# Optimization experiments

Measured on AMD Instinct MI355X. Metric: run time of the kernel, lower is better.

## Reference

```python
import jax, jax.numpy as jnp
import numpy as np

BINS = 2048
SCENE = 8
EPS = 1e-8
P_LOW = 2.0
P_HIGH = 100.0


def setup_inputs() -> dict:
    key = jax.random.key(0)
    k1, k2 = jax.random.split(key)
    x = jax.random.uniform(k1, (8, 1, 1024, 1280), dtype=jnp.float32)
    delta = jax.random.normal(k2, (SCENE, BINS), dtype=jnp.float32)
    return {"x": x, "delta": delta}


def reference(x, delta):
    B = x.shape[0]
    if x.shape[1] == 3:
        x = jnp.mean(x, axis=1, keepdims=True)
    # robust per-sample quantile normalization -> [0, 1]
    x_flat = x.reshape(B, -1)
    lo = jnp.quantile(x_flat, P_LOW / 100.0, axis=1).reshape(B, 1, 1, 1)
    hi = jnp.quantile(x_flat, P_HIGH / 100.0, axis=1).reshape(B, 1, 1, 1)
    xn = jnp.clip((x - lo) / (hi - lo + EPS), 0.0, 1.0)
    # uniform scene mixture (scene selector unused in original forward)
    scene_idx = jnp.ones((B, SCENE), dtype=x.dtype) / SCENE
    increments = jax.nn.softplus(scene_idx @ delta) + EPS  # (B, BINS)
    luts = jnp.cumsum(increments, axis=1)
    luts = luts / (luts[:, -1:] + EPS) * 2.0 - 1.0  # monotonic, range ~[-1, 1]
    # per-sample gather: pixel value -> bin index -> LUT value
    idx = jnp.clip((xn * (BINS - 1)).astype(jnp.int32), 0, BINS - 1)  # (B,1,H,W)
    y = jnp.take_along_axis(luts, idx.reshape(B, -1), axis=1).reshape(xn.shape)
    return jnp.tile(y, (1, 3, 1, 1))
```

## Files before the change

kernel.cpp:

```cpp
#include <hip/hip_runtime.h>
#include <hip/hip_bf16.h>
#include <math.h>

#define NB 8
#define HH 1024
#define WW 1280
#define HW (HH*WW)
#define N4 (HW/4)
#define LBINS 2048
#define HBINS 2048
#define NSCENE 8
#define EPSF 1e-8f
#define CAPMAX 8192

typedef float f32x4 __attribute__((ext_vector_type(4)));

#define WS_HIST    0
#define WS_MAXB    (WS_HIST + NB*HBINS)
#define WS_CNT     (WS_MAXB + NB)
#define WS_ZERO_WORDS (WS_CNT + NB)
#define WS_INFO    16400
#define WS_LOHI    (WS_INFO + NB*4)
#define WS_LUT     (WS_LOHI + NB*2)
#define WS_COLLECT 18560

__device__ __forceinline__ unsigned fkey(float f) {
    unsigned u = __float_as_uint(f);
    return (u & 0x80000000u) ? ~u : (u | 0x80000000u);
}
__device__ __forceinline__ float keyf(unsigned k) {
    unsigned u = (k & 0x80000000u) ? (k & 0x7fffffffu) : ~k;
    return __uint_as_float(u);
}

__global__ __launch_bounds__(256) void k_zero(unsigned* __restrict__ ws) {
    int i = blockIdx.x * 256 + threadIdx.x;
    if (i < WS_ZERO_WORDS) ws[i] = 0u;
}

__global__ __launch_bounds__(256) void k_hist(const float* __restrict__ x,
                                              unsigned* __restrict__ ws) {
    __shared__ unsigned lh[HBINS];
    __shared__ float redf[4];
    const int s = blockIdx.y;
    for (int i = threadIdx.x; i < HBINS; i += 256) lh[i] = 0u;
    __syncthreads();
    const float4* xs = (const float4*)(x + (size_t)s * HW);
    float mx = -3.4e38f;
    for (int i = blockIdx.x * 256 + threadIdx.x; i < N4; i += gridDim.x * 256) {
        float4 v = xs[i];
        float fv[4] = {v.x, v.y, v.z, v.w};
#pragma unroll
        for (int c = 0; c < 4; ++c) {
            float f = fv[c];
            int b = (int)(f * 2048.0f);
            b = b < 0 ? 0 : (b > 2047 ? 2047 : b);
            atomicAdd(&lh[b], 1u);
            mx = fmaxf(mx, f);
        }
    }
    for (int d = 32; d > 0; d >>= 1) mx = fmaxf(mx, __shfl_down(mx, d));
    __syncthreads();
    if ((threadIdx.x & 63) == 0) redf[threadIdx.x >> 6] = mx;
    __syncthreads();
    unsigned* gh = ws + WS_HIST + s * HBINS;
    for (int i = threadIdx.x; i < HBINS; i += 256) {
        unsigned c = lh[i];
        if (c) atomicAdd(&gh[i], c);
    }
    if (threadIdx.x == 0) {
        float m2 = fmaxf(fmaxf(redf[0], redf[1]), fmaxf(redf[2], redf[3]));
        atomicMax(&ws[WS_MAXB + s], fkey(m2));
    }
}

__global__ __launch_bounds__(64) void k_scan(unsigned* __restrict__ ws) {
    const int s = blockIdx.x;
    const unsigned* gh = ws + WS_HIST + s * HBINS;
    int lane = threadIdx.x;
    unsigned cnt[32];
    unsigned run = 0u;
#pragma unroll
    for (int i = 0; i < 32; ++i) { cnt[i] = gh[lane * 32 + i]; run += cnt[i]; }
    unsigned xs = run;
    for (int d = 1; d < 64; d <<= 1) {
        unsigned y = __shfl_up(xs, d);
        if (lane >= d) xs += y;
    }
    unsigned before = xs - run;
    const float idxf = 0.02f * (float)(HW - 1);
    const unsigned k = (unsigned)idxf;
#pragma unroll
    for (int i = 0; i < 32; ++i) {
        unsigned c = cnt[i];
        unsigned bin = lane * 32 + i;
        if (before <= k && k < before + c) {
            ws[WS_INFO + s * 4 + 0] = bin;
            ws[WS_INFO + s * 4 + 2] = k - before;
        }
        if (before <= k + 1 && k + 1 < before + c) {
            ws[WS_INFO + s * 4 + 1] = bin;
        }
        before += c;
    }
}

__global__ __launch_bounds__(64) void k_lut(const float* __restrict__ delta,
                                            float* __restrict__ lut) {
    __shared__ float inc[LBINS];
    int lane = threadIdx.x;
    for (int j = lane; j < LBINS; j += 64) {
        float ssum = 0.0f;
#pragma unroll
        for (int sc = 0; sc < NSCENE; ++sc) ssum += delta[sc * LBINS + j];
        float v = ssum * 0.125f;
        inc[j] = fmaxf(v, 0.0f) + log1pf(expf(-fabsf(v))) + EPSF;
    }
    __syncthreads();
    float loc[32];
    float run = 0.0f;
#pragma unroll
    for (int i = 0; i < 32; ++i) { run += inc[lane * 32 + i]; loc[i] = run; }
    float xv = run;
    for (int d = 1; d < 64; d <<= 1) {
        float y = __shfl_up(xv, d);
        if (lane >= d) xv += y;
    }
    float excl = xv - run;
    float total = __shfl(xv, 63);
#pragma unroll
    for (int i = 0; i < 32; ++i) {
        float c = excl + loc[i];
        lut[lane * 32 + i] = c / (total + EPSF) * 2.0f - 1.0f;
    }
}

__global__ __launch_bounds__(256) void k_collect(const float* __restrict__ x,
                                                 unsigned* __restrict__ ws, int cap) {
    const int s = blockIdx.y;
    const unsigned t1 = ws[WS_INFO + s * 4 + 0];
    const unsigned t2 = ws[WS_INFO + s * 4 + 1];
    float* coll = (float*)(ws + WS_COLLECT) + (size_t)s * cap;
    unsigned* cnt = ws + WS_CNT + s;
    const float4* xs = (const float4*)(x + (size_t)s * HW);
    for (int i = blockIdx.x * 256 + threadIdx.x; i < N4; i += gridDim.x * 256) {
        float4 v = xs[i];
        float fv[4] = {v.x, v.y, v.z, v.w};
#pragma unroll
        for (int c = 0; c < 4; ++c) {
            float f = fv[c];
            int b = (int)(f * 2048.0f);
            b = b < 0 ? 0 : (b > 2047 ? 2047 : b);
            if ((unsigned)b >= t1 && (unsigned)b <= t2) {
                unsigned p = atomicAdd(cnt, 1u);
                if (p < (unsigned)cap) coll[p] = f;
            }
        }
    }
}

__global__ __launch_bounds__(256) void k_select(unsigned* __restrict__ ws, int cap) {
    __shared__ unsigned keys[CAPMAX];
    __shared__ unsigned hist[256];
    __shared__ unsigned pfx[256];
    __shared__ unsigned s_bucket, s_r;
    __shared__ unsigned s_L, s_E, s_mg;
    const int s = blockIdx.x;
    const int tid = threadIdx.x;
    unsigned m = ws[WS_CNT + s];
    if (m > (unsigned)cap) m = (unsigned)cap;
    const float* coll = (const float*)(ws + WS_COLLECT) + (size_t)s * cap;
    const unsigned jrel = ws[WS_INFO + s * 4 + 2];

    for (unsigned i = tid; i < m; i += 256) keys[i] = fkey(coll[i]);
    if (tid == 0) { s_L = 0; s_E = 0; s_mg = 0xFFFFFFFFu; }
    __syncthreads();

    unsigned prefix = 0;
    unsigned r = jrel;
    for (int shift = 24; shift >= 0; shift -= 8) {
        hist[tid] = 0u;
        __syncthreads();
        for (unsigned i = tid; i < m; i += 256) {
            unsigned kk = keys[i];
            bool ok = (shift == 24) || ((kk >> (shift + 8)) == prefix);
            if (ok) atomicAdd(&hist[(kk >> shift) & 255u], 1u);
        }
        __syncthreads();
        if (tid < 64) {
            unsigned a0 = hist[tid*4+0], a1 = hist[tid*4+1];
            unsigned a2 = hist[tid*4+2], a3 = hist[tid*4+3];
            unsigned sum = a0 + a1 + a2 + a3;
            unsigned inc = sum;
            for (int d = 1; d < 64; d <<= 1) {
                unsigned y = __shfl_up(inc, d);
                if (tid >= d) inc += y;
            }
            unsigned excl = inc - sum;
            pfx[tid*4+0] = excl;
            pfx[tid*4+1] = excl + a0;
            pfx[tid*4+2] = excl + a0 + a1;
            pfx[tid*4+3] = excl + a0 + a1 + a2;
        }
        __syncthreads();
        {
            unsigned e = pfx[tid], c = hist[tid];
            if (e <= r && r < e + c) { s_bucket = tid; s_r = r - e; }
        }
        __syncthreads();
        prefix = (prefix << 8) | s_bucket;
        r = s_r;
        __syncthreads();
    }
    const unsigned vk = prefix;
    unsigned lL = 0, lE = 0, lmg = 0xFFFFFFFFu;
    for (unsigned i = tid; i < m; i += 256) {
        unsigned kk = keys[i];
        lL += (kk < vk) ? 1u : 0u;
        lE += (kk == vk) ? 1u : 0u;
        if (kk > vk && kk < lmg) lmg = kk;
    }
    atomicAdd(&s_L, lL);
    atomicAdd(&s_E, lE);
    atomicMin(&s_mg, lmg);
    __syncthreads();
    if (tid == 0) {
        unsigned vk1 = (jrel + 1 < s_L + s_E) ? vk : s_mg;
        float svk = keyf(vk), svk1 = keyf(vk1);
        const float idxf = 0.02f * (float)(HW - 1);
        const float frac = idxf - (float)((unsigned)idxf);
        float lo = svk * (1.0f - frac) + svk1 * frac;
        float hi = keyf(ws[WS_MAXB + s]);
        float* lh = (float*)(ws + WS_LOHI);
        lh[s * 2 + 0] = lo;
        lh[s * 2 + 1] = hi;
    }
}

__global__ __launch_bounds__(256) void k_apply(const float* __restrict__ x,
                                               const unsigned* __restrict__ ws,
                                               float* __restrict__ y) {
    __shared__ float slut[LBINS];
    const float* lutg = (const float*)(ws + WS_LUT);
    for (int i = threadIdx.x; i < LBINS; i += 256) slut[i] = lutg[i];
    const int s = blockIdx.y;
    const float* lh = (const float*)(ws + WS_LOHI);
    const float lo = lh[s * 2 + 0];
    const float hi = lh[s * 2 + 1];
    const float denom = hi - lo + EPSF;
    __syncthreads();
    const f32x4* xs = (const f32x4*)(x + (size_t)s * HW);
    f32x4* y0 = (f32x4*)(y + (size_t)s * 3 * HW);
    f32x4* y1 = (f32x4*)(y + (size_t)s * 3 * HW + HW);
    f32x4* y2 = (f32x4*)(y + (size_t)s * 3 * HW + 2 * HW);
    for (int i = blockIdx.x * 256 + threadIdx.x; i < N4; i += gridDim.x * 256) {
        f32x4 v = xs[i];
        f32x4 o;
#pragma unroll
        for (int c = 0; c < 4; ++c) {
            float xn = (v[c] - lo) / denom;
            xn = xn < 0.0f ? 0.0f : (xn > 1.0f ? 1.0f : xn);
            float t = xn * 2047.0f;
            int idx = (int)t;
            idx = idx < 0 ? 0 : (idx > 2047 ? 2047 : idx);
            o[c] = slut[idx];
        }
        __builtin_nontemporal_store(o, &y0[i]);
        __builtin_nontemporal_store(o, &y1[i]);
        __builtin_nontemporal_store(o, &y2[i]);
    }
}

extern "C" void kernel_launch(void* const* d_in, const int* in_sizes, int n_in,
                              void* d_out, int out_size, void* d_ws, size_t ws_size,
                              hipStream_t stream) {
    const float* x = (const float*)d_in[0];
    const float* delta = (const float*)d_in[1];
    float* y = (float*)d_out;
    unsigned* ws = (unsigned*)d_ws;

    int cap = CAPMAX;
    size_t avail_words = ws_size / 4;
    size_t per_sample = avail_words > WS_COLLECT ? (avail_words - WS_COLLECT) / NB : 0;
    if ((size_t)cap > per_sample) cap = (int)per_sample;

    k_zero<<<dim3((WS_ZERO_WORDS + 255) / 256), dim3(256), 0, stream>>>(ws);
    k_hist<<<dim3(64, NB), dim3(256), 0, stream>>>(x, ws);
    k_scan<<<dim3(NB), dim3(64), 0, stream>>>(ws);
    k_lut<<<dim3(1), dim3(64), 0, stream>>>(delta, (float*)(ws + WS_LUT));
    k_collect<<<dim3(32, NB), dim3(256), 0, stream>>>(x, ws, cap);
    k_select<<<dim3(NB), dim3(256), 0, stream>>>(ws, cap);
    k_apply<<<dim3(320, NB), dim3(256), 0, stream>>>(x, ws, y);
}
```

Baseline: 300.4 us.

## Replace global histogram atomics with per-block partials and merge scan/LUT kernels

The histogram kernel now writes a per-block partial histogram and per-block max to workspace instead of atomically adding into a zeroed global histogram. That removes the zeroing kernel and the global atomics. The scan and LUT kernels are fused into one launch with an extra block for the LUT, and that kernel reduces the partials and max and resets the collect counter. The collect grid is doubled. Launch count drops by two, but the scan must now read 64 partial histograms per sample (about 4 MB in total), and the workspace layout grows.

```diff
diff --git a/kernel.cpp b/kernel.cpp
--- a/kernel.cpp
+++ b/kernel.cpp
@@ -12,17 +12,17 @@
 #define NSCENE 8
 #define EPSF 1e-8f
 #define CAPMAX 8192
+#define HBLK 64
 
 typedef float f32x4 __attribute__((ext_vector_type(4)));
 
-#define WS_HIST    0
-#define WS_MAXB    (WS_HIST + NB*HBINS)
-#define WS_CNT     (WS_MAXB + NB)
-#define WS_ZERO_WORDS (WS_CNT + NB)
-#define WS_INFO    16400
+#define WS_PART    0
+#define WS_PMAX    (WS_PART + NB*HBLK*HBINS)
+#define WS_INFO    (WS_PMAX + NB*HBLK)
 #define WS_LOHI    (WS_INFO + NB*4)
 #define WS_LUT     (WS_LOHI + NB*2)
-#define WS_COLLECT 18560
+#define WS_CNT     (WS_LUT + LBINS)
+#define WS_COLLECT (WS_CNT + NB)
 
 __device__ __forceinline__ unsigned fkey(float f) {
     unsigned u = __float_as_uint(f);
@@ -31,11 +31,6 @@
 __device__ __forceinline__ float keyf(unsigned k) {
     unsigned u = (k & 0x80000000u) ? (k & 0x7fffffffu) : ~k;
     return __uint_as_float(u);
-}
-
-__global__ __launch_bounds__(256) void k_zero(unsigned* __restrict__ ws) {
-    int i = blockIdx.x * 256 + threadIdx.x;
-    if (i < WS_ZERO_WORDS) ws[i] = 0u;
 }
 
 __global__ __launch_bounds__(256) void k_hist(const float* __restrict__ x,
@@ -47,7 +42,7 @@
     __syncthreads();
     const float4* xs = (const float4*)(x + (size_t)s * HW);
     float mx = -3.4e38f;
-    for (int i = blockIdx.x * 256 + threadIdx.x; i < N4; i += gridDim.x * 256) {
+    for (int i = blockIdx.x * 256 + threadIdx.x; i < N4; i += HBLK * 256) {
         float4 v = xs[i];
         float fv[4] = {v.x, v.y, v.z, v.w};
 #pragma unroll
@@ -60,40 +55,77 @@
         }
     }
     for (int d = 32; d > 0; d >>= 1) mx = fmaxf(mx, __shfl_down(mx, d));
-    __syncthreads();
     if ((threadIdx.x & 63) == 0) redf[threadIdx.x >> 6] = mx;
     __syncthreads();
-    unsigned* gh = ws + WS_HIST + s * HBINS;
-    for (int i = threadIdx.x; i < HBINS; i += 256) {
-        unsigned c = lh[i];
-        if (c) atomicAdd(&gh[i], c);
-    }
+    unsigned* myp = ws + WS_PART + ((size_t)s * HBLK + blockIdx.x) * HBINS;
+    for (int i = threadIdx.x; i < HBINS; i += 256) myp[i] = lh[i];
     if (threadIdx.x == 0) {
         float m2 = fmaxf(fmaxf(redf[0], redf[1]), fmaxf(redf[2], redf[3]));
-        atomicMax(&ws[WS_MAXB + s], fkey(m2));
-    }
-}
-
-__global__ __launch_bounds__(64) void k_scan(unsigned* __restrict__ ws) {
+        ((float*)(ws + WS_PMAX))[s * HBLK + blockIdx.x] = m2;
+    }
+}
+
+__global__ __launch_bounds__(256) void k_scan_lut(unsigned* __restrict__ ws,
+                                                  const float* __restrict__ delta) {
+    __shared__ unsigned su[256];
+    __shared__ float sf[256];
     const int s = blockIdx.x;
-    const unsigned* gh = ws + WS_HIST + s * HBINS;
-    int lane = threadIdx.x;
-    unsigned cnt[32];
+    const int tid = threadIdx.x;
+    if (s == NB) {
+        float inc[8];
+        float run = 0.0f;
+#pragma unroll
+        for (int i = 0; i < 8; ++i) {
+            int j = tid * 8 + i;
+            float ssum = 0.0f;
+#pragma unroll
+            for (int sc = 0; sc < NSCENE; ++sc) ssum += delta[sc * LBINS + j];
+            float v = ssum * 0.125f;
+            run += fmaxf(v, 0.0f) + log1pf(expf(-fabsf(v))) + EPSF;
+            inc[i] = run;
+        }
+        sf[tid] = run;
+        __syncthreads();
+        for (int d = 1; d < 256; d <<= 1) {
+            float add = (tid >= d) ? sf[tid - d] : 0.0f;
+            __syncthreads();
+            sf[tid] += add;
+            __syncthreads();
+        }
+        float excl = sf[tid] - run;
+        float total = sf[255];
+        float* lut = (float*)(ws + WS_LUT);
+#pragma unroll
+        for (int i = 0; i < 8; ++i)
+            lut[tid * 8 + i] = (excl + inc[i]) / (total + EPSF) * 2.0f - 1.0f;
+        return;
+    }
+    const unsigned* part = ws + WS_PART + (size_t)s * HBLK * HBINS;
+    unsigned cnt[8];
     unsigned run = 0u;
 #pragma unroll
-    for (int i = 0; i < 32; ++i) { cnt[i] = gh[lane * 32 + i]; run += cnt[i]; }
-    unsigned xs = run;
-    for (int d = 1; d < 64; d <<= 1) {
-        unsigned y = __shfl_up(xs, d);
-        if (lane >= d) xs += y;
-    }
-    unsigned before = xs - run;
+    for (int i = 0; i < 8; ++i) {
+        int j = tid * 8 + i;
+        unsigned c = 0;
+        for (int b = 0; b < HBLK; ++b) c += part[b * HBINS + j];
+        cnt[i] = c;
+        run += c;
+    }
+    su[tid] = run;
+    __syncthreads();
+    for (int d = 1; d < 256; d <<= 1) {
+        unsigned add = (tid >= d) ? su[tid - d] : 0u;
+        __syncthreads();
+        su[tid] += add;
+        __syncthreads();
+    }
+    unsigned before = su[tid] - run;
     const float idxf = 0.02f * (float)(HW - 1);
     const unsigned k = (unsigned)idxf;
 #pragma unroll
-    for (int i = 0; i < 32; ++i) {
+    for (int i = 0; i < 8; ++i) {
         unsigned c = cnt[i];
-        unsigned bin = lane * 32 + i;
+        unsigned bin = tid * 8 + i;
         if (before <= k && k < before + c) {
             ws[WS_INFO + s * 4 + 0] = bin;
             ws[WS_INFO + s * 4 + 2] = k - before;
@@ -103,35 +135,13 @@
         }
         before += c;
     }
-}
-
-__global__ __launch_bounds__(64) void k_lut(const float* __restrict__ delta,
-                                            float* __restrict__ lut) {
-    __shared__ float inc[LBINS];
-    int lane = threadIdx.x;
-    for (int j = lane; j < LBINS; j += 64) {
-        float ssum = 0.0f;
-#pragma unroll
-        for (int sc = 0; sc < NSCENE; ++sc) ssum += delta[sc * LBINS + j];
-        float v = ssum * 0.125f;
-        inc[j] = fmaxf(v, 0.0f) + log1pf(expf(-fabsf(v))) + EPSF;
-    }
-    __syncthreads();
-    float loc[32];
-    float run = 0.0f;
-#pragma unroll
-    for (int i = 0; i < 32; ++i) { run += inc[lane * 32 + i]; loc[i] = run; }
-    float xv = run;
-    for (int d = 1; d < 64; d <<= 1) {
-        float y = __shfl_up(xv, d);
-        if (lane >= d) xv += y;
-    }
-    float excl = xv - run;
-    float total = __shfl(xv, 63);
-#pragma unroll
-    for (int i = 0; i < 32; ++i) {
-        float c = excl + loc[i];
-        lut[lane * 32 + i] = c / (total + EPSF) * 2.0f - 1.0f;
+    if (tid < 64) {
+        float mx = ((const float*)(ws + WS_PMAX))[s * HBLK + tid];
+        for (int d = 32; d > 0; d >>= 1) mx = fmaxf(mx, __shfl_down(mx, d));
+        if (tid == 0) {
+            ((float*)(ws + WS_LOHI))[s * 2 + 1] = mx;
+            ws[WS_CNT + s] = 0u;
+        }
     }
 }
 
@@ -229,11 +239,7 @@
         float svk = keyf(vk), svk1 = keyf(vk1);
         const float idxf = 0.02f * (float)(HW - 1);
         const float frac = idxf - (float)((unsigned)idxf);
-        float lo = svk * (1.0f - frac) + svk1 * frac;
-        float hi = keyf(ws[WS_MAXB + s]);
-        float* lh = (float*)(ws + WS_LOHI);
-        lh[s * 2 + 0] = lo;
-        lh[s * 2 + 1] = hi;
+        ((float*)(ws + WS_LOHI))[s * 2 + 0] = svk * (1.0f - frac) + svk1 * frac;
     }
 }
 
@@ -284,11 +290,9 @@
     size_t per_sample = avail_words > WS_COLLECT ? (avail_words - WS_COLLECT) / NB : 0;
     if ((size_t)cap > per_sample) cap = (int)per_sample;
 
-    k_zero<<<dim3((WS_ZERO_WORDS + 255) / 256), dim3(256), 0, stream>>>(ws);
-    k_hist<<<dim3(64, NB), dim3(256), 0, stream>>>(x, ws);
-    k_scan<<<dim3(NB), dim3(64), 0, stream>>>(ws);
-    k_lut<<<dim3(1), dim3(64), 0, stream>>>(delta, (float*)(ws + WS_LUT));
-    k_collect<<<dim3(32, NB), dim3(256), 0, stream>>>(x, ws, cap);
+    k_hist<<<dim3(HBLK, NB), dim3(256), 0, stream>>>(x, ws);
+    k_scan_lut<<<dim3(NB + 1), dim3(256), 0, stream>>>(ws, delta);
+    k_collect<<<dim3(64, NB), dim3(256), 0, stream>>>(x, ws, cap);
     k_select<<<dim3(NB), dim3(256), 0, stream>>>(ws, cap);
     k_apply<<<dim3(320, NB), dim3(256), 0, stream>>>(x, ws, y);
 }
```

Measured after the change: 298.0 us. No clear change (-0.8%).
